# Performance work log

Hardware: AMD Instinct MI355X
Metric: run time of the kernel (lower is better)

Reference implementation:

```python
import jax, jax.numpy as jnp
import numpy as np
from jax import lax

B, C, H, W = 4, 256, 64, 64
C8 = C // 8  # 32


def setup_inputs() -> dict:
    key = jax.random.key(0)
    ks = jax.random.split(key, 8)
    x = jax.random.normal(ks[0], (B, C, H, W), jnp.float32)
    # 1x1 conv weights stored as [out_ch, in_ch]
    wb = jax.random.normal(ks[1], (C8, 2 * C), jnp.float32) * 0.02
    bb = jax.random.normal(ks[2], (C8,), jnp.float32) * 0.02
    wc = jax.random.normal(ks[3], (C8, 2 * C), jnp.float32) * 0.02
    bc = jax.random.normal(ks[4], (C8,), jnp.float32) * 0.02
    wd = jax.random.normal(ks[5], (C, 2 * C), jnp.float32) * 0.02
    bd = jax.random.normal(ks[6], (C,), jnp.float32) * 0.02
    alpha = jnp.float32(0.5)  # nn.Parameter(zeros(1)) at init; nonzero for a meaningful test
    return {"x": x, "wb": wb, "bb": bb, "wc": wc, "bc": bc, "wd": wd, "bd": bd, "alpha": alpha}


def reference(x, wb, bb, wc, bc, wd, bd, alpha):
    b, c, h, w = x.shape
    n = h * w
    pad = [(0, 0), (0, 0), (1, 1), (1, 1)]
    # F.avg_pool2d(k=3, s=1, p=1) with count_include_pad=True -> window-sum / 9
    x_avg = lax.reduce_window(x, 0.0, lax.add, (1, 1, 3, 3), (1, 1, 1, 1), pad) / 9.0
    x_max = lax.reduce_window(x, -jnp.inf, lax.max, (1, 1, 3, 3), (1, 1, 1, 1), pad)
    cat = jnp.concatenate([x_avg, x_max], axis=1)  # [B, 2C, H, W]
    catf = cat.reshape(b, 2 * c, n)                # [B, 2C, N]
    # 1x1 convs == per-pixel linear projections
    feat_b = jnp.einsum('oc,bcn->bon', wb, catf) + bb[None, :, None]  # [B, C8, N]
    feat_c = jnp.einsum('oc,bcn->bon', wc, catf) + bc[None, :, None]  # [B, C8, N]
    feat_d = jnp.einsum('oc,bcn->bon', wd, catf) + bd[None, :, None]  # [B, C,  N]
    # attention_s = softmax(feat_b^T @ feat_c) over last dim -> [B, N, N]
    attn = jax.nn.softmax(jnp.einsum('bon,bom->bnm', feat_b, feat_c), axis=-1)
    # feat_e = feat_d @ attn^T -> [B, C, N]
    feat_e = jnp.einsum('bcn,bmn->bcm', feat_d, attn).reshape(b, c, h, w)
    return alpha * feat_e + (1.0 - alpha) * x
```

## Files before the change

### kernel.cpp

```cpp
#include <hip/hip_runtime.h>
#include <hip/hip_bf16.h>

typedef __hip_bfloat16 bf16;
typedef __attribute__((ext_vector_type(8))) short s8v;
typedef __attribute__((ext_vector_type(4))) float f4v;

__device__ __forceinline__ ushort f2u(float f) {
    bf16 h = __float2bfloat16(f);
    return *(ushort*)&h;
}


__global__ __launch_bounds__(256) void wcvt_kernel(
    const float* __restrict__ wb, const float* __restrict__ wc,
    const float* __restrict__ wd, ushort* __restrict__ Wf) {
    int f = blockIdx.x * 4 + (threadIdx.x >> 6);
    int l = threadIdx.x & 63;
    int ot = f % 20, kc = f / 20;
    int o = ot * 16 + (l & 15);
    int k0 = kc * 32 + (l >> 4) * 8;
    const float* wr = (o < 32) ? wb + (size_t)o * 512
                    : (o < 64) ? wc + (size_t)(o - 32) * 512
                               : wd + (size_t)(o - 64) * 512;
    float4 f0 = *(const float4*)(wr + k0);
    float4 f1 = *(const float4*)(wr + k0 + 4);
    ushort tmp[8] = {f2u(f0.x), f2u(f0.y), f2u(f0.z), f2u(f0.w),
                     f2u(f1.x), f2u(f1.y), f2u(f1.z), f2u(f1.w)};
    *(uint4*)(Wf + kc * 10240 + ot * 512 + l * 8) = *(uint4*)tmp;
}

__global__ __launch_bounds__(512, 2) void fused_kernel(
    const float* __restrict__ x, const ushort* __restrict__ Wf,
    const float* __restrict__ bb, const float* __restrict__ bc,
    const float* __restrict__ bd,
    ushort* __restrict__ Qb, ushort* __restrict__ Kb, ushort* __restrict__ Vf) {
    __shared__ __align__(16) char smem[117248];
    float*  Xs   = (float*)smem;
    ushort* Vls  = (ushort*)smem;
    ushort* catS = (ushort*)(smem + 50688);

    int tid = threadIdx.x;
    int bid = blockIdx.x;
    int lb = (bid & 7) * 32 + (bid >> 3);
    int b = lb >> 6, h = lb & 63;
    bool hasU = (h > 0), hasD = (h < 63);

    float4 xr[6];
#define LOADCG(CG)                                                              \
    {                                                                           \
        _Pragma("unroll")                                                       \
        for (int pp = 0; pp < 6; ++pp) {                                        \
            int linear = pp * 512 + tid;                                        \
            int w4 = linear & 15, cs_s = (linear >> 4) & 63, dh = linear >> 10; \
            int hh = h + dh - 1;                                                \
            float4 fv = {0.f, 0.f, 0.f, 0.f};                                   \
            if ((unsigned)hh < 64u)                                             \
                fv = *(const float4*)(x + ((size_t)(b * 256 + (CG) * 64 + cs_s)) * 4096 \
                                      + hh * 64 + w4 * 4);                      \
            xr[pp] = fv;                                                        \
        }                                                                       \
    }
    LOADCG(0)
    #pragma unroll
    for (int cg = 0; cg < 4; ++cg) {
        #pragma unroll
        for (int pp = 0; pp < 6; ++pp) {
            int linear = pp * 512 + tid;
            int w4 = linear & 15, cs_s = (linear >> 4) & 63, dh = linear >> 10;
            float* xp = Xs + (dh * 64 + w4 * 4) * 66 + cs_s;
            xp[0]   = xr[pp].x;
            xp[66]  = xr[pp].y;
            xp[132] = xr[pp].z;
            xp[198] = xr[pp].w;
        }
        __syncthreads();
        if (cg == 0) LOADCG(1)
        else if (cg == 1) LOADCG(2)
        else if (cg == 2) LOADCG(3)
        {
            int cs = tid & 63, wsw = tid >> 6;
            float vs[10], vm[10];
            #pragma unroll
            for (int j = 0; j < 10; ++j) {
                int w = wsw * 8 - 1 + j;
                if ((unsigned)w < 64u) {
                    float u = Xs[w * 66 + cs];
                    float m = Xs[(64 + w) * 66 + cs];
                    float d = Xs[(128 + w) * 66 + cs];
                    vs[j] = u + m + d;
                    float mx = m;
                    if (hasU) mx = fmaxf(mx, u);
                    if (hasD) mx = fmaxf(mx, d);
                    vm[j] = mx;
                } else { vs[j] = 0.f; vm[j] = -3.4e38f; }
            }
            int chb = cg * 64 + cs;
            #pragma unroll
            for (int i = 0; i < 8; ++i) {
                float sum = vs[i] + vs[i + 1] + vs[i + 2];
                float mx  = fmaxf(fmaxf(vm[i], vm[i + 1]), vm[i + 2]);
                catS[(wsw * 8 + i) * 520 + chb]       = f2u(sum * (1.f / 9.f));
                catS[(wsw * 8 + i) * 520 + 256 + chb] = f2u(mx);
            }
        }
        __syncthreads();
    }
#undef LOADCG

    int l = tid & 63, w = tid >> 6;
    int lm = l & 15, q = l >> 4;
    int nc = w & 3, oh = w >> 2;
    f4v pacc[10];
    #pragma unroll
    for (int ot = 0; ot < 10; ++ot)
        #pragma unroll
        for (int i = 0; i < 4; ++i) pacc[ot][i] = 0.f;

    const ushort* wfp = Wf + (oh * 10) * 512 + l * 8;
    const ushort* ap  = catS + (nc * 16 + lm) * 520 + q * 8;
    #pragma unroll 2
    for (int kci = 0; kci < 16; ++kci) {
        s8v Af = *(const s8v*)(ap + kci * 32);
        s8v Bf[10];
        #pragma unroll
        for (int ot = 0; ot < 10; ++ot)
            Bf[ot] = *(const s8v*)(wfp + kci * 10240 + ot * 512);
        #pragma unroll
        for (int ot = 0; ot < 10; ++ot)
            pacc[ot] = __builtin_amdgcn_mfma_f32_16x16x32_bf16(Af, Bf[ot], pacc[ot], 0, 0, 0);
    }

    size_t nrow = (size_t)((b << 12) + h * 64 + nc * 16 + q * 4);
    if (oh == 0) {
        #pragma unroll
        for (int ot = 0; ot < 2; ++ot) {
            int o = ot * 16 + lm;
            float bias = bb[o];
            #pragma unroll
            for (int r = 0; r < 4; ++r)
                Qb[(nrow + r) * 32 + o] = f2u(pacc[ot][r] + bias);
        }
        #pragma unroll
        for (int ot = 2; ot < 4; ++ot) {
            int o = ot * 16 + lm - 32;
            float bias = bc[o];
            #pragma unroll
            for (int r = 0; r < 4; ++r)
                Kb[(nrow + r) * 32 + o] = f2u(pacc[ot][r] + bias);
        }
        #pragma unroll
        for (int ot = 4; ot < 10; ++ot) {
            int c = ot * 16 + lm - 64;
            float bias = bd[c];
            ushort tmp[4];
            #pragma unroll
            for (int r = 0; r < 4; ++r) tmp[r] = f2u(pacc[ot][r] + bias);
            *(uint2*)&Vls[c * 72 + nc * 16 + q * 4] = *(uint2*)tmp;
        }
    } else {
        #pragma unroll
        for (int ot = 0; ot < 10; ++ot) {
            int c = 96 + ot * 16 + lm;
            float bias = bd[c];
            ushort tmp[4];
            #pragma unroll
            for (int r = 0; r < 4; ++r) tmp[r] = f2u(pacc[ot][r] + bias);
            *(uint2*)&Vls[c * 72 + nc * 16 + q * 4] = *(uint2*)tmp;
        }
    }
    __syncthreads();
    {
        size_t vb = ((size_t)b << 20) + (size_t)(h * 2) * 8192 + l * 8;
        #pragma unroll
        for (int i = 0; i < 2; ++i) {
            int cb = w * 2 + i;
            #pragma unroll
            for (int nh = 0; nh < 2; ++nh)
                *(uint4*)(Vf + vb + nh * 8192 + cb * 512)
                    = *(const uint4*)&Vls[(cb * 16 + lm) * 72 + nh * 32 + q * 8];
        }
    }
}

__global__ __launch_bounds__(512, 2) void attn_kernel(
    const ushort* __restrict__ Qb, const ushort* __restrict__ Kb,
    const ushort* __restrict__ Vf, const float* __restrict__ x,
    const float* __restrict__ alphap, float* __restrict__ out) {
    __shared__ __align__(16) ushort Ps[2][64][132];
    __shared__ float Lpart[4][64];
    __shared__ float Lrow[64];
    int tid = threadIdx.x;
    int l = tid & 63, w = tid >> 6;
    int lm = l & 15, q = l >> 4;
    int bid = blockIdx.x;
    int xcd = bid & 7;
    int b = xcd & 3;
    int midx = (bid >> 3) + ((xcd >> 2) << 5);
    int m0 = midx << 6;
    size_t bN = (size_t)b << 12;

    bool isS = (w < 4);
    int nsw = w & 3;

    s8v Qf[4];
    s8v kfA[2], kfB[2];
    float La[4] = {0.f, 0.f, 0.f, 0.f};
    f4v acc[4][4];
    s8v vf[16];

    const ushort* kbp = Kb + (bN + nsw * 32 + lm) * 32 + q * 8;
    const ushort* vfp = Vf + ((size_t)b << 20) + (nsw * 4) * 512 + l * 8;

    if (isS) {
        #pragma unroll
        for (int h = 0; h < 4; ++h)
            Qf[h] = *(const s8v*)(Qb + (bN + m0 + h * 16 + lm) * 32 + q * 8);
        s8v k00 = *(const s8v*)(kbp);
        s8v k01 = *(const s8v*)(kbp + 512);
        kfB[0] = *(const s8v*)(kbp + 4096);
        kfB[1] = *(const s8v*)(kbp + 4096 + 512);
        #pragma unroll
        for (int c = 0; c < 2; ++c) {
            s8v kc = c ? k01 : k00;
            #pragma unroll
            for (int h = 0; h < 4; ++h) {
                f4v S = {0.f, 0.f, 0.f, 0.f};
                S = __builtin_amdgcn_mfma_f32_16x16x32_bf16(kc, Qf[h], S, 0, 0, 0);
                ushort e[4];
                #pragma unroll
                for (int r = 0; r < 4; ++r) {
                    float f = __expf(fminf(S[r], 60.f));
                    La[h] += f; e[r] = f2u(f);
                }
                *(uint2*)&Ps[0][h * 16 + lm][nsw * 32 + c * 16 + q * 4] = *(uint2*)e;
            }
        }
    } else {
        #pragma unroll
        for (int mt = 0; mt < 4; ++mt)
            #pragma unroll
            for (int ct = 0; ct < 4; ++ct)
                #pragma unroll
                for (int i = 0; i < 4; ++i) acc[mt][ct][i] = 0.f;
        #pragma unroll
        for (int i = 0; i < 16; ++i)
            vf[i] = *(const s8v*)(vfp + (i >> 2) * 8192 + (i & 3) * 512);
    }
    __syncthreads();

#define PHASE(TT, KFS, KFP)                                                       \
    {                                                                             \
        int p = (TT) & 1;                                                         \
        if (isS) {                                                                \
            if ((TT) < 30) {                                                      \
                const ushort* kn = kbp + (size_t)((TT) + 2) * 4096;               \
                KFP[0] = *(const s8v*)kn;                                         \
                KFP[1] = *(const s8v*)(kn + 512);                                 \
            }                                                                     \
            if ((TT) < 31) {                                                      \
                _Pragma("unroll")                                                 \
                for (int c = 0; c < 2; ++c) {                                     \
                    _Pragma("unroll")                                             \
                    for (int h = 0; h < 4; ++h) {                                 \
                        f4v S = {0.f, 0.f, 0.f, 0.f};                             \
                        S = __builtin_amdgcn_mfma_f32_16x16x32_bf16(              \
                                KFS[c], Qf[h], S, 0, 0, 0);                       \
                        ushort e[4];                                              \
                        _Pragma("unroll")                                         \
                        for (int r = 0; r < 4; ++r) {                             \
                            float f = __expf(fminf(S[r], 60.f));                  \
                            La[h] += f; e[r] = f2u(f);                            \
                        }                                                         \
                        *(uint2*)&Ps[1 - p][h * 16 + lm][nsw * 32 + c * 16 + q * 4] \
                            = *(uint2*)e;                                         \
                    }                                                             \
                }                                                                 \
            }                                                                     \
        } else {                                                                  \
            const ushort* vn = vfp + (size_t)((TT) + 1) * 32768;                  \
            _Pragma("unroll")                                                     \
            for (int ks = 0; ks < 4; ++ks) {                                      \
                s8v Af[4];                                                        \
                _Pragma("unroll")                                                 \
                for (int mt = 0; mt < 4; ++mt)                                    \
                    Af[mt] = *(const s8v*)&Ps[p][mt * 16 + lm][ks * 32 + q * 8];  \
                _Pragma("unroll")                                                 \
                for (int ct = 0; ct < 4; ++ct) {                                  \
                    _Pragma("unroll")                                             \
                    for (int mt = 0; mt < 4; ++mt)                                \
                        acc[mt][ct] = __builtin_amdgcn_mfma_f32_16x16x32_bf16(    \
                            Af[mt], vf[ks * 4 + ct], acc[mt][ct], 0, 0, 0);       \
                }                                                                 \
                if ((TT) < 31) {                                                  \
                    _Pragma("unroll")                                             \
                    for (int ct = 0; ct < 4; ++ct)                                \
                        vf[ks * 4 + ct] = *(const s8v*)(vn + ks * 8192 + ct * 512); \
                }                                                                 \
            }                                                                     \
        }                                                                         \
        asm volatile("s_waitcnt lgkmcnt(0)\n\ts_barrier" ::: "memory");           \
    }

    for (int t = 0; t < 32; t += 2) {
        PHASE(t,     kfB, kfA);
        PHASE(t + 1, kfA, kfB);
    }
#undef PHASE

    if (isS) {
        #pragma unroll
        for (int h = 0; h < 4; ++h) {
            La[h] += __shfl_xor(La[h], 16, 64);
            La[h] += __shfl_xor(La[h], 32, 64);
        }
        if (q == 0) {
            #pragma unroll
            for (int h = 0; h < 4; ++h)
                Lpart[nsw][h * 16 + lm] = La[h];
        }
    }
    __syncthreads();
    if (tid < 64)
        Lrow[tid] = Lpart[0][tid] + Lpart[1][tid] + Lpart[2][tid] + Lpart[3][tid];
    __syncthreads();
    if (!isS) {
        float alpha = alphap[0];
        float ra = 1.f - alpha;
        #pragma unroll
        for (int mt = 0; mt < 4; ++mt) {
            float L0 = Lrow[mt * 16 + q * 4 + 0];
            float L1 = Lrow[mt * 16 + q * 4 + 1];
            float L2 = Lrow[mt * 16 + q * 4 + 2];
            float L3 = Lrow[mt * 16 + q * 4 + 3];
            #pragma unroll
            for (int ct = 0; ct < 4; ++ct) {
                int cc = nsw * 64 + ct * 16 + lm;
                size_t base = ((size_t)(b * 256 + cc)) * 4096 + m0 + mt * 16 + q * 4;
                float4 xv = *(const float4*)(x + base);
                float4 ov;
                ov.x = alpha * (acc[mt][ct][0] / L0) + ra * xv.x;
                ov.y = alpha * (acc[mt][ct][1] / L1) + ra * xv.y;
                ov.z = alpha * (acc[mt][ct][2] / L2) + ra * xv.z;
                ov.w = alpha * (acc[mt][ct][3] / L3) + ra * xv.w;
                *(float4*)(out + base) = ov;
            }
        }
    }
}

extern "C" void kernel_launch(void* const* d_in, const int* in_sizes, int n_in,
                              void* d_out, int out_size, void* d_ws, size_t ws_size,
                              hipStream_t stream) {
    const float* x  = (const float*)d_in[0];
    const float* wb = (const float*)d_in[1];
    const float* bb = (const float*)d_in[2];
    const float* wc = (const float*)d_in[3];
    const float* bc = (const float*)d_in[4];
    const float* wd = (const float*)d_in[5];
    const float* bd = (const float*)d_in[6];
    const float* al = (const float*)d_in[7];
    float* out = (float*)d_out;

    char* ws = (char*)d_ws;
    ushort* Qb = (ushort*)ws;
    ushort* Kb = (ushort*)(ws + 1048576);
    ushort* Vf = (ushort*)(ws + 2097152);
    ushort* Wf = (ushort*)(ws + 10485760);

    wcvt_kernel<<<dim3(80), dim3(256), 0, stream>>>(wb, wc, wd, Wf);
    fused_kernel<<<dim3(256), dim3(512), 0, stream>>>(x, Wf, bb, bc, bd,
                                                      Qb, Kb, Vf);
    attn_kernel<<<dim3(256), dim3(512), 0, stream>>>(Qb, Kb, Vf, x, al, out);
}
```

Measured before the change: 155.2 us.

## Double key-tile width per phase and add MFMA priority in attention pipeline

Each pipeline phase now processes a 256-key tile instead of 128, which halves the number of phases and block-wide barriers. The score warps compute and exponentiate four 16-key chunks per phase, and the P buffer in shared memory grows to 260 columns. The PV warps stream V through a rotating four-slot register ring with prefetch interleaved across eight k-steps, and raise wave priority with s_setprio around the MFMA bursts. The cost is more LDS (roughly double the P buffer, which may affect occupancy at 2 blocks per CU) and more register pressure from the larger key fragments.

```diff
diff --git a/kernel.cpp b/kernel.cpp
--- a/kernel.cpp
+++ b/kernel.cpp
@@ -186,7 +186,7 @@
     const ushort* __restrict__ Qb, const ushort* __restrict__ Kb,
     const ushort* __restrict__ Vf, const float* __restrict__ x,
     const float* __restrict__ alphap, float* __restrict__ out) {
-    __shared__ __align__(16) ushort Ps[2][64][132];
+    __shared__ __align__(16) ushort Ps[2][64][260];
     __shared__ float Lpart[4][64];
     __shared__ float Lrow[64];
     int tid = threadIdx.x;
@@ -203,36 +203,35 @@
     int nsw = w & 3;
 
     s8v Qf[4];
-    s8v kfA[2], kfB[2];
+    s8v kfA[4], kfB[4];
     float La[4] = {0.f, 0.f, 0.f, 0.f};
     f4v acc[4][4];
     s8v vf[16];
 
-    const ushort* kbp = Kb + (bN + nsw * 32 + lm) * 32 + q * 8;
+    const ushort* kbp = Kb + (bN + nsw * 64 + lm) * 32 + q * 8;
     const ushort* vfp = Vf + ((size_t)b << 20) + (nsw * 4) * 512 + l * 8;
 
     if (isS) {
         #pragma unroll
         for (int h = 0; h < 4; ++h)
             Qf[h] = *(const s8v*)(Qb + (bN + m0 + h * 16 + lm) * 32 + q * 8);
-        s8v k00 = *(const s8v*)(kbp);
-        s8v k01 = *(const s8v*)(kbp + 512);
-        kfB[0] = *(const s8v*)(kbp + 4096);
-        kfB[1] = *(const s8v*)(kbp + 4096 + 512);
-        #pragma unroll
-        for (int c = 0; c < 2; ++c) {
-            s8v kc = c ? k01 : k00;
+        #pragma unroll
+        for (int c = 0; c < 4; ++c) kfA[c] = *(const s8v*)(kbp + c * 512);
+        #pragma unroll
+        for (int c = 0; c < 4; ++c) kfB[c] = *(const s8v*)(kbp + 8192 + c * 512);
+        #pragma unroll
+        for (int c = 0; c < 4; ++c) {
             #pragma unroll
             for (int h = 0; h < 4; ++h) {
                 f4v S = {0.f, 0.f, 0.f, 0.f};
-                S = __builtin_amdgcn_mfma_f32_16x16x32_bf16(kc, Qf[h], S, 0, 0, 0);
+                S = __builtin_amdgcn_mfma_f32_16x16x32_bf16(kfA[c], Qf[h], S, 0, 0, 0);
                 ushort e[4];
                 #pragma unroll
                 for (int r = 0; r < 4; ++r) {
                     float f = __expf(fminf(S[r], 60.f));
                     La[h] += f; e[r] = f2u(f);
                 }
-                *(uint2*)&Ps[0][h * 16 + lm][nsw * 32 + c * 16 + q * 4] = *(uint2*)e;
+                *(uint2*)&Ps[0][h * 16 + lm][nsw * 64 + c * 16 + q * 4] = *(uint2*)e;
             }
         }
     } else {
@@ -252,14 +251,14 @@
     {                                                                             \
         int p = (TT) & 1;                                                         \
         if (isS) {                                                                \
-            if ((TT) < 30) {                                                      \
-                const ushort* kn = kbp + (size_t)((TT) + 2) * 4096;               \
-                KFP[0] = *(const s8v*)kn;                                         \
-                KFP[1] = *(const s8v*)(kn + 512);                                 \
+            if ((TT) < 14) {                                                      \
+                const ushort* kn = kbp + (size_t)((TT) + 2) * 8192;               \
+                _Pragma("unroll")                                                 \
+                for (int c = 0; c < 4; ++c) KFP[c] = *(const s8v*)(kn + c * 512); \
             }                                                                     \
-            if ((TT) < 31) {                                                      \
+            if ((TT) < 15) {                                                      \
                 _Pragma("unroll")                                                 \
-                for (int c = 0; c < 2; ++c) {                                     \
+                for (int c = 0; c < 4; ++c) {                                     \
                     _Pragma("unroll")                                             \
                     for (int h = 0; h < 4; ++h) {                                 \
                         f4v S = {0.f, 0.f, 0.f, 0.f};                             \
@@ -271,37 +270,41 @@
                             float f = __expf(fminf(S[r], 60.f));                  \
                             La[h] += f; e[r] = f2u(f);                            \
                         }                                                         \
-                        *(uint2*)&Ps[1 - p][h * 16 + lm][nsw * 32 + c * 16 + q * 4] \
+                        *(uint2*)&Ps[1 - p][h * 16 + lm][nsw * 64 + c * 16 + q * 4] \
                             = *(uint2*)e;                                         \
                     }                                                             \
                 }                                                                 \
             }                                                                     \
         } else {                                                                  \
-            const ushort* vn = vfp + (size_t)((TT) + 1) * 32768;                  \
+            const ushort* vbase = vfp + (size_t)(TT) * 65536;                     \
             _Pragma("unroll")                                                     \
-            for (int ks = 0; ks < 4; ++ks) {                                      \
+            for (int s = 0; s < 8; ++s) {                                         \
+                int slot = s & 3;                                                 \
                 s8v Af[4];                                                        \
                 _Pragma("unroll")                                                 \
                 for (int mt = 0; mt < 4; ++mt)                                    \
-                    Af[mt] = *(const s8v*)&Ps[p][mt * 16 + lm][ks * 32 + q * 8];  \
+                    Af[mt] = *(const s8v*)&Ps[p][mt * 16 + lm][s * 32 + q * 8];   \
+                __builtin_amdgcn_s_setprio(1);                                    \
                 _Pragma("unroll")                                                 \
                 for (int ct = 0; ct < 4; ++ct) {                                  \
                     _Pragma("unroll")                                             \
                     for (int mt = 0; mt < 4; ++mt)                                \
                         acc[mt][ct] = __builtin_amdgcn_mfma_f32_16x16x32_bf16(    \
-                            Af[mt], vf[ks * 4 + ct], acc[mt][ct], 0, 0, 0);       \
+                            Af[mt], vf[slot * 4 + ct], acc[mt][ct], 0, 0, 0);     \
                 }                                                                 \
-                if ((TT) < 31) {                                                  \
+                __builtin_amdgcn_s_setprio(0);                                    \
+                if (s < 4 || (TT) < 15) {                                         \
+                    const ushort* vn = vbase + (size_t)(s + 4) * 8192;            \
                     _Pragma("unroll")                                             \
                     for (int ct = 0; ct < 4; ++ct)                                \
-                        vf[ks * 4 + ct] = *(const s8v*)(vn + ks * 8192 + ct * 512); \
+                        vf[slot * 4 + ct] = *(const s8v*)(vn + ct * 512);         \
                 }                                                                 \
             }                                                                     \
         }                                                                         \
         asm volatile("s_waitcnt lgkmcnt(0)\n\ts_barrier" ::: "memory");           \
     }
 
-    for (int t = 0; t < 32; t += 2) {
+    for (int t = 0; t < 16; t += 2) {
         PHASE(t,     kfB, kfA);
         PHASE(t + 1, kfA, kfB);
     }
```

Result: faster. 151.6 us (-2.3%).
